# Performance work log

Hardware: AMD Instinct MI355X
Metric: run time of the kernel (lower is better)

Reference implementation:

```python
import jax, jax.numpy as jnp
import numpy as np

N_BATCH = 2; N_RAYS = 4096; S_COARSE = 32; S_FINE = 32
FEATURE_DIM = 32; BOX_WARP = 6.0; EPS = 1e-5

_PLANE_AXES = np.array([[[1, 0, 0], [0, 1, 0], [0, 0, 1]],
                        [[1, 0, 0], [0, 0, 1], [0, 1, 0]],
                        [[0, 0, 1], [0, 1, 0], [1, 0, 0]]], dtype=np.float32)
_INV_PLANES = np.linalg.inv(_PLANE_AXES)  # [3,3,3]


def _grid_sample(feat, coords):
    # feat [B,C,H,W], coords [B,M,2] in [-1,1] (x->W, y->H); bilinear, align_corners=False, zero padding
    B, C, H, W = feat.shape
    x = (coords[..., 0] + 1.0) * (W * 0.5) - 0.5
    y = (coords[..., 1] + 1.0) * (H * 0.5) - 0.5
    x0 = jnp.floor(x); y0 = jnp.floor(y)
    wx = x - x0; wy = y - y0
    x0i = x0.astype(jnp.int32); y0i = y0.astype(jnp.int32)

    def corner(fb, yi, xi):
        valid = ((xi >= 0) & (xi < W) & (yi >= 0) & (yi < H)).astype(fb.dtype)
        v = fb[:, jnp.clip(yi, 0, H - 1), jnp.clip(xi, 0, W - 1)]  # [C,M]
        return v * valid[None, :]

    def one(fb, x0b, y0b, wxb, wyb):
        x1b = x0b + 1; y1b = y0b + 1
        return (corner(fb, y0b, x0b) * (1 - wxb) * (1 - wyb)
                + corner(fb, y0b, x1b) * wxb * (1 - wyb)
                + corner(fb, y1b, x0b) * (1 - wxb) * wyb
                + corner(fb, y1b, x1b) * wxb * wyb)  # [C,M]

    return jax.vmap(one)(feat, x0i, y0i, wx, wy)  # [B,C,M]


def _sample_from_planes(planes, coords):
    # planes [N,3,C,H,W], coords [N,M,3] -> [N,3,M,C]
    N, n_planes, C, H, W = planes.shape
    M = coords.shape[1]
    c = coords * (2.0 / BOX_WARP)
    proj = jnp.einsum('nmc,pcd->npmd', c, jnp.asarray(_INV_PLANES))[..., :2]  # [N,3,M,2]
    out = _grid_sample(planes.reshape(N * n_planes, C, H, W), proj.reshape(N * n_planes, M, 2))
    return out.reshape(N, n_planes, C, M).transpose(0, 1, 3, 2)


def _decoder(feat, W1, b1, W2, b2):
    # OSGDecoder: Linear -> softplus -> Linear; rgb sigmoid-squashed, sigma raw
    h = jax.nn.softplus(feat @ W1 + b1)
    o = h @ W2 + b2
    rgb = jax.nn.sigmoid(o[..., 1:]) * (1 + 2 * 0.001) - 0.001
    sigma = o[..., 0:1]
    return rgb, sigma


def _run_model(planes, coords, W1, b1, W2, b2, beta):
    sf = _sample_from_planes(planes, coords).mean(axis=1)  # [N,M,C]
    rgb, raw_sigma = _decoder(sf, W1, b1, W2, b2)
    pred_sdf = raw_sigma
    # template SDF stand-in (external FLAME tex_feature net): sphere SDF
    tsdf = jnp.linalg.norm(coords, axis=-1, keepdims=True) - 0.5
    sigma = raw_sigma + tsdf
    density = jax.nn.sigmoid(-sigma / beta) / beta  # sdf_activation(-sigma)
    return rgb, density, pred_sdf


def _ray_march(colors, densities, depths):
    deltas = depths[:, :, 1:] - depths[:, :, :-1]
    c_mid = 0.5 * (colors[:, :, :-1] + colors[:, :, 1:])
    d_mid = 0.5 * (densities[:, :, :-1] + densities[:, :, 1:])
    z_mid = 0.5 * (depths[:, :, :-1] + depths[:, :, 1:])
    alpha = 1.0 - jnp.exp(-d_mid * deltas)
    shifted = jnp.concatenate([jnp.ones_like(alpha[:, :, :1]), 1.0 - alpha + 1e-10], axis=2)
    weights = alpha * jnp.cumprod(shifted, axis=2)[:, :, :-1]
    comp_rgb = jnp.sum(weights * c_mid, axis=2) * 2.0 - 1.0
    w_tot = jnp.sum(weights, axis=2)
    comp_depth = jnp.sum(weights * z_mid, axis=2) / w_tot
    comp_depth = jnp.nan_to_num(comp_depth, nan=jnp.inf)
    comp_depth = jnp.clip(comp_depth, depths.min(), depths.max())
    return comp_rgb, comp_depth, weights


def _sample_pdf(bins, weights, u):
    n_w = weights.shape[-1]
    w = weights + EPS
    pdf = w / jnp.sum(w, axis=-1, keepdims=True)
    cdf = jnp.cumsum(pdf, axis=-1)
    cdf = jnp.concatenate([jnp.zeros_like(cdf[:, :1]), cdf], axis=-1)
    inds = jax.vmap(lambda c, uu: jnp.searchsorted(c, uu, side='right'))(cdf, u)
    below = jnp.maximum(inds - 1, 0)
    above = jnp.minimum(inds, n_w)
    cdf0 = jnp.take_along_axis(cdf, below, axis=-1)
    cdf1 = jnp.take_along_axis(cdf, above, axis=-1)
    b0 = jnp.take_along_axis(bins, below, axis=-1)
    b1v = jnp.take_along_axis(bins, above, axis=-1)
    denom = cdf1 - cdf0
    denom = jnp.where(denom < EPS, 1.0, denom)
    return b0 + (u - cdf0) / denom * (b1v - b0)


def _sample_importance(z_vals, weights, u):
    B, R, S, _ = z_vals.shape
    z = z_vals.reshape(B * R, S)
    w = weights.reshape(B * R, -1)  # S-1
    # torch max_pool1d(k=2,s=1,pad=1) then avg_pool1d(k=2,s=1)
    neg = jnp.full_like(w[:, :1], -1e10)
    wp = jnp.concatenate([neg, w, neg], axis=-1)
    m = jnp.maximum(wp[:, :-1], wp[:, 1:])  # len S
    w_sm = 0.5 * (m[:, :-1] + m[:, 1:]) + 0.01  # len S-1
    z_mid = 0.5 * (z[:, :-1] + z[:, 1:])  # len S-1
    s = _sample_pdf(z_mid, w_sm[:, 1:-1], u)
    return jax.lax.stop_gradient(s.reshape(B, R, -1, 1))


def reference(planes, ray_origins, ray_directions, hit_min_depth, hit_max_depth, jitter, u_importance, W1, b1, W2, b2, sigmoid_beta, hit_mask):
    N, M, _ = ray_origins.shape
    beta = jnp.maximum(sigmoid_beta, 0.002)
    mask = hit_mask.astype(planes.dtype)[:, :, None, None]  # [N,M,1,1]
    hmin = jnp.where(mask == 0, hit_min_depth.min(), hit_min_depth)
    hmax = jnp.where(mask == 0, hit_max_depth.max(), hit_max_depth)
    base = jnp.linspace(0.0, 1.0, S_COARSE, dtype=planes.dtype).reshape(1, 1, S_COARSE, 1)
    span = hmax - hmin
    d_coarse = (base + jitter * span / S_COARSE) * span + hmin  # [N,M,S,1]

    def eval_points(depths):
        coords = ray_origins[:, :, None, :] + depths * ray_directions[:, :, None, :]
        S = depths.shape[2]
        rgb, dens, psdf = _run_model(planes, coords.reshape(N, M * S, 3), W1, b1, W2, b2, beta)
        # masked scatter-back into dense buffers == multiply by hit mask
        rgb = rgb.reshape(N, M, S, FEATURE_DIM) * mask
        dens = dens.reshape(N, M, S, 1) * mask
        return rgb, dens, psdf

    rgb_c, dens_c, psdf_c = eval_points(d_coarse)
    _, _, w_c = _ray_march(rgb_c, dens_c, d_coarse)
    d_fine = _sample_importance(d_coarse, w_c, u_importance)
    rgb_f, dens_f, psdf_f = eval_points(d_fine)

    all_d = jnp.concatenate([d_coarse, d_fine], axis=2)
    all_c = jnp.concatenate([rgb_c, rgb_f], axis=2)
    all_s = jnp.concatenate([dens_c, dens_f], axis=2)
    idx = jnp.argsort(all_d, axis=2)
    all_d = jnp.take_along_axis(all_d, idx, axis=2)
    all_c = jnp.take_along_axis(all_c, jnp.broadcast_to(idx, all_c.shape), axis=2)
    all_s = jnp.take_along_axis(all_s, jnp.broadcast_to(idx, all_s.shape), axis=2)

    rgb_final, depth_final, weights = _ray_march(all_c, all_s, all_d)
    all_pred_sdf = jnp.concatenate([psdf_c, psdf_f], axis=1)
    return rgb_final, depth_final, weights, all_pred_sdf


def setup_inputs():
    key = jax.random.key(0)
    ks = jax.random.split(key, 12)
    planes = jax.random.normal(ks[0], (N_BATCH, 3, 32, 256, 256), jnp.float32)
    ray_origins = 0.1 * jax.random.normal(ks[1], (N_BATCH, N_RAYS, 3), jnp.float32)
    rd = jax.random.normal(ks[2], (N_BATCH, N_RAYS, 3), jnp.float32)
    ray_directions = rd / jnp.linalg.norm(rd, axis=-1, keepdims=True)
    hit_min_depth = 0.8 + 0.4 * jax.random.uniform(ks[3], (N_BATCH, N_RAYS, 1, 1), jnp.float32)
    hit_max_depth = hit_min_depth + 0.5 + jax.random.uniform(ks[4], (N_BATCH, N_RAYS, 1, 1), jnp.float32)
    jitter = jax.random.uniform(ks[5], (N_BATCH, N_RAYS, S_COARSE, 1), jnp.float32)
    u_importance = jax.random.uniform(ks[6], (N_BATCH * N_RAYS, S_FINE), jnp.float32)
    W1 = 0.05 * jax.random.normal(ks[7], (32, 64), jnp.float32)
    b1 = jnp.zeros((64,), jnp.float32)
    W2 = 0.05 * jax.random.normal(ks[8], (64, 1 + FEATURE_DIM), jnp.float32)
    b2 = jnp.zeros((1 + FEATURE_DIM,), jnp.float32)
    sigmoid_beta = 0.1 * jnp.ones((1,), jnp.float32)
    hit_mask = jax.random.randint(ks[9], (N_BATCH, N_RAYS), 0, 2, jnp.int32)
    return {'planes': planes, 'ray_origins': ray_origins, 'ray_directions': ray_directions,
            'hit_min_depth': hit_min_depth, 'hit_max_depth': hit_max_depth, 'jitter': jitter,
            'u_importance': u_importance, 'W1': W1, 'b1': b1, 'W2': W2, 'b2': b2,
            'sigmoid_beta': sigmoid_beta, 'hit_mask': hit_mask}
```

## Files before the change

### kernel.cpp

```cpp
#include <hip/hip_runtime.h>
#include <hip/hip_bf16.h>
#include <math.h>
#include <stddef.h>

typedef unsigned int u32;
typedef unsigned short u16;
typedef unsigned long long u64;

#define NRAYS 8192
#define NSAMP 262144

__device__ __forceinline__ float fa(float a,float b){ return __fadd_rn(a,b); }
__device__ __forceinline__ float fs(float a,float b){ return __fsub_rn(a,b); }
__device__ __forceinline__ float fm(float a,float b){ return __fmul_rn(a,b); }
__device__ __forceinline__ float fdv(float a,float b){ return __fdiv_rn(a,b); }

__device__ __forceinline__ double exp_d(double x){
  const double LOG2E  = 1.4426950408889634074;
  const double LN2_HI = 6.93147180369123816490e-01;
  const double LN2_LO = 1.90821492927058770002e-10;
  double kd = rint(x * LOG2E);
  if (kd >  200.0) return INFINITY;
  if (kd < -200.0) return 0.0;
  int k = (int)kd;
  double r = fma(-kd, LN2_HI, x);
  r = fma(-kd, LN2_LO, r);
  double p = 1.0/39916800.0;
  p = fma(p, r, 1.0/3628800.0);
  p = fma(p, r, 1.0/362880.0);
  p = fma(p, r, 1.0/40320.0);
  p = fma(p, r, 1.0/5040.0);
  p = fma(p, r, 1.0/720.0);
  p = fma(p, r, 1.0/120.0);
  p = fma(p, r, 1.0/24.0);
  p = fma(p, r, 1.0/6.0);
  p = fma(p, r, 0.5);
  p = fma(p, r, 1.0);
  p = fma(p, r, 1.0);
  u64 sb = ((u64)(k + 1023)) << 52;
  return p * __longlong_as_double((long long)sb);
}
__device__ __forceinline__ double log1p_d(double y){
  double s = y / (2.0 + y);
  double s2 = s*s;
  double p = 2.0/29.0;
  p = fma(p, s2, 2.0/27.0);
  p = fma(p, s2, 2.0/25.0);
  p = fma(p, s2, 2.0/23.0);
  p = fma(p, s2, 2.0/21.0);
  p = fma(p, s2, 2.0/19.0);
  p = fma(p, s2, 2.0/17.0);
  p = fma(p, s2, 2.0/15.0);
  p = fma(p, s2, 2.0/13.0);
  p = fma(p, s2, 2.0/11.0);
  p = fma(p, s2, 2.0/9.0);
  p = fma(p, s2, 2.0/7.0);
  p = fma(p, s2, 2.0/5.0);
  p = fma(p, s2, 2.0/3.0);
  p = fma(p, s2, 2.0);
  return p * s;
}
__device__ __forceinline__ float exf(float x){ return (float)exp_d((double)x); }
__device__ __forceinline__ float l1pf_(float x){ return (float)log1p_d((double)x); }
__device__ __forceinline__ float sigm(float x){
  if (x >= 0.f){ float e = exf(-x); return fdv(1.f, fa(1.f, e)); }
  float e = exf(x); return fdv(e, fa(1.f, e));
}
__device__ __forceinline__ float sigm_fast(float x){
  return 1.f/(1.f + __expf(-x));
}
__device__ __forceinline__ u16 f2b(float f){
  u32 x = __float_as_uint(f);
  return (u16)((x + 0x7fffu + ((x>>16)&1u)) >> 16);
}
__device__ __forceinline__ u32 fenc(float f){ u32 b=__float_as_uint(f); return (b&0x80000000u)? ~b : (b|0x80000000u); }
__device__ __forceinline__ float fdec(u32 k){ u32 b=(k&0x80000000u)? (k^0x80000000u) : ~k; return __uint_as_float(b); }

__global__ void k_init(const float* __restrict__ hmin, const float* __restrict__ hmax,
                       const float* __restrict__ W1, float* __restrict__ scal,
                       float* __restrict__ W1t){
  __shared__ float smn[256], smx[256];
  int t = threadIdx.x;
  float mn = 1e30f, mx = -1e30f;
  for (int i=t;i<NRAYS;i+=256){ mn=fminf(mn,hmin[i]); mx=fmaxf(mx,hmax[i]); }
  smn[t]=mn; smx[t]=mx; __syncthreads();
  for(int s=128;s>0;s>>=1){
    if(t<s){ smn[t]=fminf(smn[t],smn[t+s]); smx[t]=fmaxf(smx[t],smx[t+s]); }
    __syncthreads();
  }
  if(t==0){
    scal[0]=smn[0]; scal[1]=smx[0];
    ((u32*)scal)[2]=0xFFFFFFFFu;
    ((u32*)scal)[3]=0u;
  }
  for(int i=t;i<2048;i+=256){ int j=i>>5, c=i&31; W1t[i]=W1[c*64+j]; }
}

__global__ void __launch_bounds__(256) k_tr(const float* __restrict__ pl, float* __restrict__ pt){
  int t = blockIdx.x*256 + threadIdx.x;
  int x  = t & 255;
  int c4 = ((t>>8)&7)<<2;
  int y  = (t>>11)&255;
  int np = t>>19;
  const float* ip = pl + (((size_t)(np*32+c4))<<16) + (y<<8) + x;
  float4 o;
  o.x = ip[0];
  o.y = ip[65536];
  o.z = ip[131072];
  o.w = ip[196608];
  *reinterpret_cast<float4*>(pt + ((((size_t)(np<<8|y))<<8|x)<<5) + c4) = o;
}

template<int PHASE>
__global__ void __launch_bounds__(256) k_eval(
  const float* __restrict__ pt, const float* __restrict__ ro, const float* __restrict__ rd,
  const float* __restrict__ hmin, const float* __restrict__ hmax,
  const float* __restrict__ jitter, const int* __restrict__ hitmask,
  const float* __restrict__ W1t, const float* __restrict__ b1,
  const float* __restrict__ W2, const float* __restrict__ b2,
  const float* __restrict__ sb, float* __restrict__ scal,
  float* __restrict__ dep, float* __restrict__ dens_out, u16* __restrict__ rgb_out,
  float* __restrict__ out_psdf)
{
  int idx = blockIdx.x*256 + threadIdx.x;
  int ray = idx >> 5;
  int s   = idx & 31;
  int n   = ray >> 12;
  int msk = hitmask[ray];

  float d;
  if (PHASE==0){
    float hmn = msk ? hmin[ray] : scal[0];
    float hmx = msk ? hmax[ray] : scal[1];
    float span = fs(hmx, hmn);
    float jit  = jitter[idx];
    float base = (float)((double)s * (1.0/31.0));
    if (s==31) base = 1.0f;
    float t1 = fdv(fm(jit, span), 32.0f);
    d = fa(fm(fa(base, t1), span), hmn);
    dep[idx] = d;
    float dm=d, dM=d;
#pragma unroll
    for (int m=1;m<64;m<<=1){ dm=fminf(dm,__shfl_xor(dm,m)); dM=fmaxf(dM,__shfl_xor(dM,m)); }
    if ((threadIdx.x & 63)==0){
      atomicMin(((u32*)scal)+2, fenc(dm));
      atomicMax(((u32*)scal)+3, fenc(dM));
    }
  } else {
    d = dep[idx];
  }

  float ox=ro[ray*3+0], oy=ro[ray*3+1], oz=ro[ray*3+2];
  float dx=rd[ray*3+0], dy=rd[ray*3+1], dz=rd[ray*3+2];
  float px = fa(ox, fm(d,dx)), py = fa(oy, fm(d,dy)), pz = fa(oz, fm(d,dz));
  float nrm = __fsqrt_rn(fa(fa(fm(px,px),fm(py,py)),fm(pz,pz)));
  float tsdf = fs(nrm, 0.5f);
  const float sc2 = (float)(2.0/6.0);
  float cx=fm(px,sc2), cy=fm(py,sc2), cz=fm(pz,sc2);

  float feat[32];
#pragma unroll
  for(int c=0;c<32;c++) feat[c]=0.f;

#pragma unroll
  for (int p=0;p<3;p++){
    float u = (p==2)?cz:cx;
    float v = (p==1)?cz:cy;
    float fx = fs(fm(fa(u,1.f),128.f),0.5f);
    float fy = fs(fm(fa(v,1.f),128.f),0.5f);
    float x0f = floorf(fx), y0f = floorf(fy);
    float wx = fs(fx,x0f), wy = fs(fy,y0f);
    float ax0 = fs(1.f,wx), ax1 = wx, ay0 = fs(1.f,wy), ay1 = wy;
    int x0, y0;
    {
      x0 = (x0f >= 2.1e9f) ? 2147483647 : ((x0f <= -2.1e9f) ? (-2147483647-1) : (int)x0f);
      y0 = (y0f >= 2.1e9f) ? 2147483647 : ((y0f <= -2.1e9f) ? (-2147483647-1) : (int)y0f);
    }
    int x1=x0+1, y1=y0+1;
    bool vx0 = (x0>=0 && x0<256), vx1 = (x1>=0 && x1<256);
    bool vy0 = (y0>=0 && y0<256), vy1 = (y1>=0 && y1<256);
    bool ok00 = vx0&&vy0, ok01 = vx1&&vy0, ok10 = vx0&&vy1, ok11 = vx1&&vy1;
    int cx0=min(max(x0,0),255), cx1=min(max(x1,0),255);
    int cy0=min(max(y0,0),255), cy1=min(max(y1,0),255);
    int npl = n*3+p;
    size_t pb = ((size_t)npl)<<16;
    const float4* t00 = (const float4*)(pt + ((pb + (cy0<<8) + cx0)<<5));
    const float4* t01 = (const float4*)(pt + ((pb + (cy0<<8) + cx1)<<5));
    const float4* t10 = (const float4*)(pt + ((pb + (cy1<<8) + cx0)<<5));
    const float4* t11 = (const float4*)(pt + ((pb + (cy1<<8) + cx1)<<5));
#pragma unroll
    for(int q=0;q<8;q++){
      float4 v00 = t00[q], v01 = t01[q], v10 = t10[q], v11 = t11[q];
      float e0,e1,e2,e3, t_;
#define CORNER_SUM(FLD, OUTI) \
      e0 = ok00 ? v00.FLD : 0.f; e1 = ok01 ? v01.FLD : 0.f; \
      e2 = ok10 ? v10.FLD : 0.f; e3 = ok11 ? v11.FLD : 0.f; \
      t_ = fa(fa(fa(fm(fm(e0,ax0),ay0), fm(fm(e1,ax1),ay0)), fm(fm(e2,ax0),ay1)), fm(fm(e3,ax1),ay1)); \
      feat[q*4+OUTI] = fa(feat[q*4+OUTI], t_);
      CORNER_SUM(x,0) CORNER_SUM(y,1) CORNER_SUM(z,2) CORNER_SUM(w,3)
#undef CORNER_SUM
    }
  }
#pragma unroll
  for(int c=0;c<32;c++) feat[c] = fdv(feat[c], 3.0f);

  float o[33];
#pragma unroll
  for(int k=0;k<33;k++) o[k]=0.f;
#pragma unroll 2
  for(int j=0;j<64;j++){
    float a = 0.f;
#pragma unroll
    for(int c=0;c<32;c++) a = fmaf(feat[c], W1t[j*32+c], a);
    a = fa(a, b1[j]);
    float h = fa(fmaxf(a,0.f), l1pf_(exf(-fabsf(a))));
#pragma unroll
    for(int k=0;k<33;k++) o[k] = fmaf(h, W2[j*33+k], o[k]);
  }
#pragma unroll
  for(int k=0;k<33;k++) o[k] = fa(o[k], b2[k]);

  float beta = fmaxf(sb[0], 0.002f);
  float raw = o[0];
  out_psdf[((size_t)n<<18) + ((size_t)PHASE<<17) + (size_t)(ray&4095)*32 + s] = raw;
  float sg = fa(raw, tsdf);
  float dens = msk ? fdv(sigm(fdv(-sg, beta)), beta) : 0.f;
  dens_out[idx]=dens;

  u16 rv[32];
#pragma unroll
  for(int c=0;c<32;c++){
    float r = msk ? fs(fm(sigm_fast(o[c+1]), 1.002f), 0.001f) : 0.f;
    rv[c]=f2b(r);
  }
  uint4* op = (uint4*)(rgb_out + (size_t)idx*32);
#pragma unroll
  for(int q=0;q<4;q++){
    uint4 w;
    w.x = (u32)rv[q*8+0] | ((u32)rv[q*8+1]<<16);
    w.y = (u32)rv[q*8+2] | ((u32)rv[q*8+3]<<16);
    w.z = (u32)rv[q*8+4] | ((u32)rv[q*8+5]<<16);
    w.w = (u32)rv[q*8+6] | ((u32)rv[q*8+7]<<16);
    op[q]=w;
  }
}

__global__ void __launch_bounds__(64) k_imp(
  const float* __restrict__ dc, const float* __restrict__ dens,
  const float* __restrict__ u_imp, float* __restrict__ df, float* __restrict__ scal)
{
  __shared__ float scdf[64][30];
  __shared__ float szm [64][30];
  int tid = threadIdx.x;
  int ray = blockIdx.x*64 + tid;
  float w[31];
  float dprev = dc[ray*32+0];
  float sprev = dens[ray*32+0];
  float T = 1.f;
#pragma unroll
  for(int i=0;i<31;i++){
    float dn = dc[ray*32+i+1];
    float sn = dens[ray*32+i+1];
    if (i<30) szm[tid][i] = fm(0.5f, fa(dprev,dn));
    float delta = fs(dn,dprev);
    float dm = fm(0.5f, fa(sprev,sn));
    float al = fs(1.f, exf(-fm(dm,delta)));
    w[i] = fm(al,T);
    T = fm(T, fa(fs(1.f,al), 1e-10f));
    dprev=dn; sprev=sn;
  }
  float pdfw[29];
#pragma unroll
  for(int i=0;i<29;i++){
    float m1 = fmaxf(w[i],w[i+1]), m2 = fmaxf(w[i+1],w[i+2]);
    pdfw[i] = fa(fa(fm(0.5f, fa(m1,m2)), 0.01f), 1e-5f);
  }
  float sum;
  {
    float r[8];
#pragma unroll
    for(int j=0;j<8;j++) r[j]=pdfw[j];
#pragma unroll
    for(int j=0;j<8;j++) r[j]=fa(r[j],pdfw[8+j]);
#pragma unroll
    for(int j=0;j<8;j++) r[j]=fa(r[j],pdfw[16+j]);
    sum = fa(fa(fa(r[0],r[1]),fa(r[2],r[3])), fa(fa(r[4],r[5]),fa(r[6],r[7])));
#pragma unroll
    for(int i=24;i<29;i++) sum = fa(sum, pdfw[i]);
  }
  {
    float cacc = 0.f;
    scdf[tid][0] = 0.f;
#pragma unroll
    for(int i=1;i<30;i++){
      cacc = fa(cacc, fdv(pdfw[i-1], sum));
      scdf[tid][i] = cacc;
    }
  }

  float fmn=1e30f, fmx=-1e30f;
  for(int k=0;k<32;k++){
    float u = u_imp[ray*32+k];
    int lo=0, hi=30;
    while(lo<hi){
      int mid=(lo+hi)>>1;
      if (scdf[tid][mid] <= u) lo = mid+1; else hi = mid;
    }
    int ind = lo;
    int below = ind-1;
    int above = (ind>29)?29:ind;
    float cdf0 = scdf[tid][below];
    float cdf1 = scdf[tid][above];
    float b0   = szm [tid][below];
    float b1v  = szm [tid][above];
    float den = fs(cdf1,cdf0);
    if((double)den < 1e-5) den = 1.f;
    float sres = fa(b0, fm(fdv(fs(u,cdf0),den), fs(b1v,b0)));
    df[ray*32+k]=sres;
    fmn=fminf(fmn,sres); fmx=fmaxf(fmx,sres);
  }
#pragma unroll
  for(int m=1;m<64;m<<=1){ fmn=fminf(fmn,__shfl_xor(fmn,m)); fmx=fmaxf(fmx,__shfl_xor(fmx,m)); }
  if(tid==0){
    atomicMin(((u32*)scal)+2, fenc(fmn));
    atomicMax(((u32*)scal)+3, fenc(fmx));
  }
}

__global__ void __launch_bounds__(256) k_final(
  const float* __restrict__ dc, const float* __restrict__ df,
  const float* __restrict__ densc, const float* __restrict__ densf,
  const u16* __restrict__ rgbc, const u16* __restrict__ rgbf,
  const float* __restrict__ scal,
  float* __restrict__ out_rgb, float* __restrict__ out_depth, float* __restrict__ out_w)
{
  __shared__ float ssd[4][64];
  __shared__ float ssn[4][64];
  __shared__ int   sp [4][64];
  __shared__ float swv[4][64];
  __shared__ float swz[4][64];
  int wid = threadIdx.x>>6, lane = threadIdx.x&63;
  int ray = blockIdx.x*4 + wid;

  float myd = (lane<32)? dc[ray*32+lane]    : df[ray*32+lane-32];
  float myn = (lane<32)? densc[ray*32+lane] : densf[ray*32+lane-32];
  ssd[wid][lane]=myd; __syncthreads();
  int rk=0;
#pragma unroll 8
  for(int j=0;j<64;j++){
    float dj = ssd[wid][j];
    rk += (dj<myd || (dj==myd && j<lane)) ? 1:0;
  }
  __syncthreads();
  ssd[wid][rk]=myd; ssn[wid][rk]=myn; sp[wid][rk]=lane;
  __syncthreads();

  float T=1.f, accr=0.f;
  int j0 = sp[wid][0];
  float cprev = 0.f;
  if (lane<32){
    const u16* cb = (j0<32)? (rgbc+((size_t)ray*32+j0)*32) : (rgbf+((size_t)ray*32+(j0-32))*32);
    cprev = __uint_as_float(((u32)cb[lane])<<16);
  }
  float d0 = ssd[wid][0], n0 = ssn[wid][0];
  for(int s2=0;s2<63;s2++){
    float d1 = ssd[wid][s2+1], n1 = ssn[wid][s2+1];
    float delta = fs(d1,d0);
    float dm = fm(0.5f, fa(n0,n1));
    float al = fs(1.f, exf(-fm(dm,delta)));
    float wv = fm(al,T);
    T = fm(T, fa(fs(1.f,al), 1e-10f));
    if (lane==s2){ swv[wid][s2]=wv; swz[wid][s2]=fm(wv, fm(0.5f, fa(d0,d1))); }
    int j1 = sp[wid][s2+1];
    float cnext = 0.f;
    if (lane<32){
      const u16* cb = (j1<32)? (rgbc+((size_t)ray*32+j1)*32) : (rgbf+((size_t)ray*32+(j1-32))*32);
      cnext = __uint_as_float(((u32)cb[lane])<<16);
    }
    accr = fa(accr, fm(wv, fm(0.5f, fa(cprev,cnext))));
    cprev=cnext; d0=d1; n0=n1;
  }
  __syncthreads();
  if(lane<63) out_w[(size_t)ray*63+lane]=swv[wid][lane];
  if(lane<32) out_rgb[(size_t)ray*32+lane]=fs(fm(accr,2.f),1.f);
  if(lane==0){
    float wsum, zsum;
    {
      float r[8], rz[8];
#pragma unroll
      for(int j=0;j<8;j++){ r[j]=swv[wid][j]; rz[j]=swz[wid][j]; }
      for(int i=8;i<56;i+=8)
#pragma unroll
        for(int j=0;j<8;j++){ r[j]=fa(r[j],swv[wid][i+j]); rz[j]=fa(rz[j],swz[wid][i+j]); }
      wsum = fa(fa(fa(r[0],r[1]),fa(r[2],r[3])), fa(fa(r[4],r[5]),fa(r[6],r[7])));
      zsum = fa(fa(fa(rz[0],rz[1]),fa(rz[2],rz[3])), fa(fa(rz[4],rz[5]),fa(rz[6],rz[7])));
      for(int i=56;i<63;i++){ wsum=fa(wsum,swv[wid][i]); zsum=fa(zsum,swz[wid][i]); }
    }
    float depv = fdv(zsum, wsum);
    if (isnan(depv)) depv = INFINITY;
    float lo = fdec(((const u32*)scal)[2]);
    float hi = fdec(((const u32*)scal)[3]);
    depv = fminf(fmaxf(depv,lo),hi);
    out_depth[ray]=depv;
  }
}

extern "C" void kernel_launch(void* const* d_in, const int* in_sizes, int n_in,
                              void* d_out, int out_size, void* d_ws, size_t ws_size,
                              hipStream_t stream) {
  const float* planes = (const float*)d_in[0];
  const float* ro     = (const float*)d_in[1];
  const float* rdp    = (const float*)d_in[2];
  const float* hmin   = (const float*)d_in[3];
  const float* hmax   = (const float*)d_in[4];
  const float* jitter = (const float*)d_in[5];
  const float* uimp   = (const float*)d_in[6];
  const float* W1     = (const float*)d_in[7];
  const float* b1     = (const float*)d_in[8];
  const float* W2     = (const float*)d_in[9];
  const float* b2     = (const float*)d_in[10];
  const float* sb     = (const float*)d_in[11];
  const int*   hmk    = (const int*)d_in[12];
  float* out = (float*)d_out;
  char* ws = (char*)d_ws;

  size_t off=0;
  auto alloc=[&](size_t bytes){ size_t o=off; off=(off+bytes+255)&~(size_t)255; return o; };
  float* scal = (float*)(ws+alloc(64));
  float* W1t  = (float*)(ws+alloc(2048*4));
  float* pt   = (float*)(ws+alloc((size_t)12582912*4));
  float* dco  = (float*)(ws+alloc((size_t)NSAMP*4));
  float* dfi  = (float*)(ws+alloc((size_t)NSAMP*4));
  float* dnc  = (float*)(ws+alloc((size_t)NSAMP*4));
  float* dnf  = (float*)(ws+alloc((size_t)NSAMP*4));
  u16*   rgc  = (u16*)  (ws+alloc((size_t)NSAMP*32*2));
  u16*   rgf  = (u16*)  (ws+alloc((size_t)NSAMP*32*2));
  (void)in_sizes; (void)n_in; (void)out_size; (void)ws_size;

  float* out_rgb  = out;
  float* out_dep  = out + 262144;
  float* out_w    = out + 270336;
  float* out_psdf = out + 786432;

  k_init<<<dim3(1),dim3(256),0,stream>>>(hmin,hmax,W1,scal,W1t);
  k_tr<<<dim3(12288),dim3(256),0,stream>>>(planes, pt);
  k_eval<0><<<dim3(1024),dim3(256),0,stream>>>(pt,ro,rdp,hmin,hmax,jitter,hmk,W1t,b1,W2,b2,sb,scal,dco,dnc,rgc,out_psdf);
  k_imp<<<dim3(128),dim3(64),0,stream>>>(dco,dnc,uimp,dfi,scal);
  k_eval<1><<<dim3(1024),dim3(256),0,stream>>>(pt,ro,rdp,hmin,hmax,jitter,hmk,W1t,b1,W2,b2,sb,scal,dfi,dnf,rgf,out_psdf);
  k_final<<<dim3(2048),dim3(256),0,stream>>>(dco,dfi,dnc,dnf,rgc,rgf,scal,out_rgb,out_dep,out_w);
}
```

Before: 498.7 us.

## Use float softplus math and split MLP dot product into parallel accumulators

Replaces the double-precision exp/log1p polynomial softplus in the decoder hidden layer with single-precision expf/log1pf. The layer-1 dot product is split into four independent accumulators to shorten the FMA dependency chain. The j-loop unroll is raised to 4, and launch bounds now request 4 blocks per CU. Double-precision math per hidden unit was expensive, so this mainly cuts ALU cost, at the risk of small numerical differences and register pressure from the larger unroll.

```diff
diff --git a/kernel.cpp b/kernel.cpp
--- a/kernel.cpp
+++ b/kernel.cpp
@@ -40,28 +40,7 @@
   u64 sb = ((u64)(k + 1023)) << 52;
   return p * __longlong_as_double((long long)sb);
 }
-__device__ __forceinline__ double log1p_d(double y){
-  double s = y / (2.0 + y);
-  double s2 = s*s;
-  double p = 2.0/29.0;
-  p = fma(p, s2, 2.0/27.0);
-  p = fma(p, s2, 2.0/25.0);
-  p = fma(p, s2, 2.0/23.0);
-  p = fma(p, s2, 2.0/21.0);
-  p = fma(p, s2, 2.0/19.0);
-  p = fma(p, s2, 2.0/17.0);
-  p = fma(p, s2, 2.0/15.0);
-  p = fma(p, s2, 2.0/13.0);
-  p = fma(p, s2, 2.0/11.0);
-  p = fma(p, s2, 2.0/9.0);
-  p = fma(p, s2, 2.0/7.0);
-  p = fma(p, s2, 2.0/5.0);
-  p = fma(p, s2, 2.0/3.0);
-  p = fma(p, s2, 2.0);
-  return p * s;
-}
 __device__ __forceinline__ float exf(float x){ return (float)exp_d((double)x); }
-__device__ __forceinline__ float l1pf_(float x){ return (float)log1p_d((double)x); }
 __device__ __forceinline__ float sigm(float x){
   if (x >= 0.f){ float e = exf(-x); return fdv(1.f, fa(1.f, e)); }
   float e = exf(x); return fdv(e, fa(1.f, e));
@@ -112,7 +91,7 @@
 }
 
 template<int PHASE>
-__global__ void __launch_bounds__(256) k_eval(
+__global__ void __launch_bounds__(256,4) k_eval(
   const float* __restrict__ pt, const float* __restrict__ ro, const float* __restrict__ rd,
   const float* __restrict__ hmin, const float* __restrict__ hmax,
   const float* __restrict__ jitter, const int* __restrict__ hitmask,
@@ -207,15 +186,22 @@
   float o[33];
 #pragma unroll
   for(int k=0;k<33;k++) o[k]=0.f;
-#pragma unroll 2
+#pragma unroll 4
   for(int j=0;j<64;j++){
-    float a = 0.f;
-#pragma unroll
-    for(int c=0;c<32;c++) a = fmaf(feat[c], W1t[j*32+c], a);
-    a = fa(a, b1[j]);
-    float h = fa(fmaxf(a,0.f), l1pf_(exf(-fabsf(a))));
-#pragma unroll
-    for(int k=0;k<33;k++) o[k] = fmaf(h, W2[j*33+k], o[k]);
+    const float* wr = W1t + j*32;
+    float a0=0.f, a1=0.f, a2=0.f, a3=0.f;
+#pragma unroll
+    for(int c=0;c<8;c++){
+      a0 = fmaf(feat[c   ], wr[c   ], a0);
+      a1 = fmaf(feat[c+ 8], wr[c+ 8], a1);
+      a2 = fmaf(feat[c+16], wr[c+16], a2);
+      a3 = fmaf(feat[c+24], wr[c+24], a3);
+    }
+    float a = fa(fa(fa(a0,a1),fa(a2,a3)), b1[j]);
+    float h = fa(fmaxf(a,0.f), log1pf(expf(-fabsf(a))));
+    const float* w2r = W2 + j*33;
+#pragma unroll
+    for(int k=0;k<33;k++) o[k] = fmaf(h, w2r[k], o[k]);
   }
 #pragma unroll
   for(int k=0;k<33;k++) o[k] = fa(o[k], b2[k]);
```

After: 570.3 us. +14.4%, slower.
